# Kernel tuning notes

Hardware: AMD Instinct MI355X
Metric: run time of the kernel (lower is better)

Reference implementation:

```python
import jax, jax.numpy as jnp
import numpy as np

N = 50000
E = 800000
IN_C, HID_C, OUT_C = 64, 96, 32


def setup_inputs() -> dict:
    key = jax.random.key(0)
    ks = jax.random.split(key, 8)
    x = jax.random.normal(ks[0], (N, IN_C), dtype=jnp.float32)
    edge_index = jax.random.randint(ks[1], (2, E), 0, N, dtype=jnp.int32)
    W1 = jax.random.normal(ks[2], (IN_C, HID_C), dtype=jnp.float32) / np.sqrt(IN_C)
    b1 = jnp.zeros((HID_C,), jnp.float32)
    W2 = jax.random.normal(ks[3], (HID_C, HID_C), dtype=jnp.float32) / np.sqrt(HID_C)
    b2 = jnp.zeros((HID_C,), jnp.float32)
    Wfc = jax.random.normal(ks[4], (HID_C, OUT_C), dtype=jnp.float32) / np.sqrt(HID_C)
    bfc = jnp.zeros((OUT_C,), jnp.float32)
    return {"x": x, "edge_index": edge_index, "W1": W1, "b1": b1,
            "W2": W2, "b2": b2, "Wfc": Wfc, "bfc": bfc}


def _gcn_conv(x, src, dst, norm, W, b):
    # x' = D^{-1/2}(A+I)D^{-1/2} (x W) + b   (PyG GCNConv default)
    h = x @ W                                # [N, C_out]
    msg = h[src] * norm[:, None]             # gather + edge scaling
    agg = jax.ops.segment_sum(msg, dst, num_segments=N)  # scatter-add
    return agg + b


def reference(x, edge_index, W1, b1, W2, b2, Wfc, bfc):
    loop = jnp.arange(N, dtype=edge_index.dtype)
    src = jnp.concatenate([edge_index[0], loop])  # add self-loops
    dst = jnp.concatenate([edge_index[1], loop])
    deg = jax.ops.segment_sum(jnp.ones(src.shape[0], jnp.float32), dst,
                              num_segments=N)
    dinv = jax.lax.rsqrt(deg)                # deg >= 1 due to self-loops
    norm = dinv[src] * dinv[dst]             # symmetric normalization per edge
    h = jax.nn.relu(_gcn_conv(x, src, dst, norm, W1, b1))
    # dropout omitted (eval mode / identity)
    h = jax.nn.relu(_gcn_conv(h, src, dst, norm, W2, b2))
    return h @ Wfc + bfc
```

## Files before the change

### kernel.cpp

```cpp
#include <hip/hip_runtime.h>
#include <hip/hip_fp16.h>


constexpr int NN = 50000;
constexpr int NE = 800000;
constexpr int NB = 512;
constexpr int NPB = 98;
constexpr int BCAP = 2048;
constexpr int EPB = 8192;
constexpr int P1B = 1024;
constexpr int NP1 = (NE + EPB - 1) / EPB;

__global__ void zero_bcnt(int* bcnt) {
  int i = threadIdx.x;
  if (i < NB) bcnt[i] = 0;
}

__global__ __launch_bounds__(P1B) void csr_pass1(const int* __restrict__ ei,
                                                 int* __restrict__ bcnt,
                                                 unsigned* __restrict__ bbuf) {
  __shared__ unsigned sorted[EPB];
  __shared__ int hist[NB];
  __shared__ int lofs[NB];
  __shared__ int cursor[NB];
  __shared__ int gbase[NB];
  const int t = threadIdx.x;
  const int e0 = blockIdx.x * EPB;
  const int ecnt = min(EPB, NE - e0);

  for (int i = t; i < NB; i += P1B) hist[i] = 0;
  __syncthreads();

  for (int i = t; i < ecnt; i += P1B) {
    unsigned dst = (unsigned)ei[NE + e0 + i];
    atomicAdd(&hist[dst / NPB], 1);
  }
  __syncthreads();

  if (t < NB) lofs[t] = hist[t];
  __syncthreads();
  for (int off = 1; off < NB; off <<= 1) {
    int v = 0;
    if (t < NB && t >= off) v = lofs[t - off];
    __syncthreads();
    if (t < NB) lofs[t] += v;
    __syncthreads();
  }
  if (t < NB) {
    int ex = lofs[t] - hist[t];
    lofs[t] = ex;
    cursor[t] = ex;
    gbase[t] = atomicAdd(&bcnt[t], hist[t]);
  }
  __syncthreads();

  for (int i = t; i < ecnt; i += P1B) {
    unsigned src = (unsigned)ei[e0 + i];
    unsigned dst = (unsigned)ei[NE + e0 + i];
    unsigned b = dst / NPB;
    unsigned dl = dst - b * NPB;
    int pos = atomicAdd(&cursor[b], 1);
    sorted[pos] = (b << 23) | (dl << 16) | src;
  }
  __syncthreads();

  for (int i = t; i < ecnt; i += P1B) {
    unsigned pw = sorted[i];
    unsigned b = pw >> 23;
    int off_in_b = gbase[b] + (i - lofs[b]);
    if (off_in_b < BCAP)
      bbuf[b * BCAP + off_in_b] = pw & 0x007FFFFFu;
  }
}

__global__ __launch_bounds__(256) void csr_pass2(
    const int* __restrict__ bcnt, const unsigned* __restrict__ bbuf,
    const float* __restrict__ x, int* __restrict__ row_start,
    int* __restrict__ counts, float* __restrict__ dinv,
    __half* __restrict__ u, unsigned short* __restrict__ srcs,
    unsigned* __restrict__ perm) {
  __shared__ int s_red[256];
  __shared__ int s_cnt[128];
  __shared__ int s_scan[128];
  __shared__ int s_cur[128];
  __shared__ float s_dinv[128];
  __shared__ unsigned short s_sorted[BCAP];
  __shared__ int d_hist[64];
  __shared__ int d_cur[64];
  __shared__ int s_permL[NPB];
  const int b = blockIdx.x, t = threadIdx.x;
  const int cnt_b = min(bcnt[b], BCAP);

  int acc = 0;
  for (int j = t; j < b; j += 256) acc += min(bcnt[j], BCAP);
  s_red[t] = acc;
  __syncthreads();
  for (int off = 128; off > 0; off >>= 1) {
    if (t < off) s_red[t] += s_red[t + off];
    __syncthreads();
  }
  const int base = s_red[0];

  if (t < 128) s_cnt[t] = 0;
  __syncthreads();
  for (int i = t; i < cnt_b; i += 256)
    atomicAdd(&s_cnt[bbuf[b * BCAP + i] >> 16], 1);
  __syncthreads();

  if (t < 128) s_scan[t] = s_cnt[t];
  __syncthreads();
  for (int off = 1; off < 128; off <<= 1) {
    int v = 0;
    if (t < 128 && t >= off) v = s_scan[t - off];
    __syncthreads();
    if (t < 128) s_scan[t] += v;
    __syncthreads();
  }
  if (t < 128) s_cur[t] = s_scan[t] - s_cnt[t];

  const int node = b * NPB + t;
  if (t < NPB && node < NN) {
    int c = s_cnt[t];
    row_start[node] = base + s_scan[t] - c;
    counts[node] = c;
    float di = rsqrtf(1.0f + (float)c);
    dinv[node] = di;
    s_dinv[t] = di;
  }
  __syncthreads();

  for (int i = t; i < cnt_b; i += 256) {
    unsigned w = bbuf[b * BCAP + i];
    int pos = atomicAdd(&s_cur[w >> 16], 1);
    s_sorted[pos] = (unsigned short)(w & 0xFFFFu);
  }
  __syncthreads();
  for (int i = t; i < cnt_b; i += 256) srcs[base + i] = s_sorted[i];

  const int na = max(0, min(NN - b * NPB, NPB));
  if (t < 64) d_hist[t] = 0;
  __syncthreads();
  const bool activeN = (t < na);
  const int deg = activeN ? min(s_cnt[t], 63) : 0;
  if (activeN) atomicAdd(&d_hist[deg], 1);
  __syncthreads();
  if (t < 64) d_cur[t] = d_hist[t];
  __syncthreads();
  for (int off = 1; off < 64; off <<= 1) {
    int v = 0;
    if (t < 64 && t >= off) v = d_cur[t - off];
    __syncthreads();
    if (t < 64) d_cur[t] += v;
    __syncthreads();
  }
  if (t < 64) d_cur[t] -= d_hist[t];
  __syncthreads();
  if (activeN) {
    int r = atomicAdd(&d_cur[deg], 1);
    s_permL[r] = t;
  }
  __syncthreads();
  if (t < NPB)
    perm[b * NPB + t] =
        (t < na) ? (unsigned)(b * NPB + s_permL[t]) : 0xFFFFFFFFu;

  const float4* x4 = (const float4*)x;
  for (int i = t; i < NPB * 16; i += 256) {
    int nl = i >> 4, q = i & 15;
    int n = b * NPB + nl;
    if (n < NN) {
      float di = s_dinv[nl];
      float4 v = x4[(size_t)n * 16 + q];
      __half2 h01 = __floats2half2_rn(v.x * di, v.y * di);
      __half2 h23 = __floats2half2_rn(v.z * di, v.w * di);
      uint2 pk;
      pk.x = *(unsigned*)&h01;
      pk.y = *(unsigned*)&h23;
      *(uint2*)(u + (size_t)n * 64 + 4 * q) = pk;
    }
  }
}

template <int C>
__global__ __launch_bounds__(256) void gather_h(
    const unsigned* __restrict__ perm, const int* __restrict__ row_start,
    const int* __restrict__ counts, const unsigned short* __restrict__ srcs,
    const __half* __restrict__ A, float* __restrict__ B) {
  constexpr int QP = C / 8;
  int gid = blockIdx.x * blockDim.x + threadIdx.x;
  if (gid >= NB * NPB * QP) return;
  int i, q;
  if constexpr ((QP & (QP - 1)) == 0) {
    i = gid >> 3;
    q = gid & 7;
  } else {
    i = gid / QP;
    q = gid - i * QP;
  }
  const unsigned node = perm[i];
  if (node == 0xFFFFFFFFu) return;
  const int n = (int)node;
  const uint4* A4 = (const uint4*)A + q;

  float a[8] = {};
  {
    uint4 v = A4[(size_t)n * QP];
    const __half2* h = (const __half2*)&v;
    #pragma unroll
    for (int k = 0; k < 4; ++k) {
      float2 f = __half22float2(h[k]);
      a[2 * k] = f.x;
      a[2 * k + 1] = f.y;
    }
  }
  const int s0 = row_start[n];
  const int cnt = counts[n];
  int p = 0;
  for (; p + 4 <= cnt; p += 4) {
    int sa = srcs[s0 + p + 0];
    int sb = srcs[s0 + p + 1];
    int sc = srcs[s0 + p + 2];
    int sd = srcs[s0 + p + 3];
    uint4 va = A4[(size_t)sa * QP];
    uint4 vb = A4[(size_t)sb * QP];
    uint4 vc = A4[(size_t)sc * QP];
    uint4 vd = A4[(size_t)sd * QP];
    const __half2* ha = (const __half2*)&va;
    const __half2* hb = (const __half2*)&vb;
    const __half2* hc = (const __half2*)&vc;
    const __half2* hd = (const __half2*)&vd;
    #pragma unroll
    for (int k = 0; k < 4; ++k) {
      float2 fa = __half22float2(ha[k]);
      float2 fb = __half22float2(hb[k]);
      float2 fc = __half22float2(hc[k]);
      float2 fd = __half22float2(hd[k]);
      a[2 * k] += (fa.x + fb.x) + (fc.x + fd.x);
      a[2 * k + 1] += (fa.y + fb.y) + (fc.y + fd.y);
    }
  }
  for (; p < cnt; ++p) {
    int s = srcs[s0 + p];
    uint4 v = A4[(size_t)s * QP];
    const __half2* h = (const __half2*)&v;
    #pragma unroll
    for (int k = 0; k < 4; ++k) {
      float2 f = __half22float2(h[k]);
      a[2 * k] += f.x;
      a[2 * k + 1] += f.y;
    }
  }
  float* bp = B + (size_t)n * C + 8 * q;
  *(float4*)bp = make_float4(a[0], a[1], a[2], a[3]);
  *(float4*)(bp + 4) = make_float4(a[4], a[5], a[6], a[7]);
}

template <int K, int M, int MS, int EMODE, int OH>
__global__ __launch_bounds__(256) void sgemm(
    const float* __restrict__ X, const float* __restrict__ W,
    const float* __restrict__ bias, const float* __restrict__ dinv,
    void* __restrict__ outv) {
  constexpr int NS = M / MS;
  constexpr int WQ = MS / 4;
  const int bid = blockIdx.x;
  const int chunk = (NS == 1) ? bid : bid / NS;
  const int slice = (NS == 1) ? 0 : bid - chunk * NS;
  const int c0 = slice * MS;
  const int t = threadIdx.x;
  const int nr = chunk * 256 + t;
  const bool act = nr < NN;
  const int n = act ? nr : NN - 1;

  float acc[MS] = {};
  const float4* __restrict__ xr = (const float4*)(X + (size_t)n * K);
  #pragma unroll 4
  for (int kq = 0; kq < K / 4; ++kq) {
    float4 xv = xr[kq];
    const float xk[4] = {xv.x, xv.y, xv.z, xv.w};
    #pragma unroll
    for (int c = 0; c < 4; ++c) {
      const float* __restrict__ wrow = W + (size_t)(4 * kq + c) * M + c0;
      #pragma unroll
      for (int j = 0; j < MS; ++j)
        acc[j] = fmaf(xk[c], wrow[j], acc[j]);
    }
  }

  if (act) {
    const float di = (EMODE != 3) ? dinv[n] : 0.f;
    #pragma unroll
    for (int j4 = 0; j4 < WQ; ++j4) {
      float b0 = bias[c0 + 4 * j4 + 0], b1 = bias[c0 + 4 * j4 + 1];
      float b2 = bias[c0 + 4 * j4 + 2], b3 = bias[c0 + 4 * j4 + 3];
      float a0 = acc[4 * j4 + 0], a1 = acc[4 * j4 + 1];
      float a2 = acc[4 * j4 + 2], a3 = acc[4 * j4 + 3];
      float4 r;
      if (EMODE == 1) {
        r.x = di * fmaxf(fmaf(di, a0, b0), 0.f);
        r.y = di * fmaxf(fmaf(di, a1, b1), 0.f);
        r.z = di * fmaxf(fmaf(di, a2, b2), 0.f);
        r.w = di * fmaxf(fmaf(di, a3, b3), 0.f);
      } else if (EMODE == 2) {
        r.x = fmaxf(fmaf(di, a0, b0), 0.f);
        r.y = fmaxf(fmaf(di, a1, b1), 0.f);
        r.z = fmaxf(fmaf(di, a2, b2), 0.f);
        r.w = fmaxf(fmaf(di, a3, b3), 0.f);
      } else {
        r.x = a0 + b0; r.y = a1 + b1; r.z = a2 + b2; r.w = a3 + b3;
      }
      if (OH) {
        __half2 h01 = __floats2half2_rn(r.x, r.y);
        __half2 h23 = __floats2half2_rn(r.z, r.w);
        uint2 pk;
        pk.x = *(unsigned*)&h01;
        pk.y = *(unsigned*)&h23;
        *(uint2*)((__half*)outv + (size_t)n * M + c0 + 4 * j4) = pk;
      } else {
        *(float4*)((float*)outv + (size_t)n * M + c0 + 4 * j4) = r;
      }
    }
  }
}

extern "C" void kernel_launch(void* const* d_in, const int* in_sizes, int n_in,
                              void* d_out, int out_size, void* d_ws,
                              size_t ws_size, hipStream_t stream) {
  const float* x   = (const float*)d_in[0];
  const int*   ei  = (const int*)d_in[1];
  const float* W1  = (const float*)d_in[2];
  const float* b1  = (const float*)d_in[3];
  const float* W2  = (const float*)d_in[4];
  const float* b2  = (const float*)d_in[5];
  const float* Wfc = (const float*)d_in[6];
  const float* bfc = (const float*)d_in[7];
  float* out = (float*)d_out;

  float* dinv = (float*)d_ws;
  float* R0 = dinv + 50048;
  float* R1 = R0 + (size_t)NN * 96;
  int* row_start = (int*)(R1 + (size_t)NN * 96);
  int* counts = row_start + 50048;
  int* bcnt = counts + 50048;
  unsigned short* srcs = (unsigned short*)(bcnt + 512);
  unsigned* perm = (unsigned*)(srcs + NE);
  unsigned* bbuf = (unsigned*)R1;
  __half* u_h = (__half*)R0;
  __half* g1_h = (__half*)R0;
  float* B1 = R1;
  float* B2 = R1;
  float* h2 = R0;

  zero_bcnt<<<1, 512, 0, stream>>>(bcnt);
  csr_pass1<<<NP1, P1B, 0, stream>>>(ei, bcnt, bbuf);
  csr_pass2<<<NB, 256, 0, stream>>>(bcnt, bbuf, x, row_start, counts, dinv,
                                    u_h, srcs, perm);

  constexpr int CH = (NN + 255) / 256;

  gather_h<64><<<(NB * NPB * 8 + 255) / 256, 256, 0, stream>>>(
      perm, row_start, counts, srcs, u_h, B1);
  sgemm<64, 96, 32, 1, 1><<<CH * 3, 256, 0, stream>>>(B1, W1, b1, dinv, g1_h);
  gather_h<96><<<(NB * NPB * 12 + 255) / 256, 256, 0, stream>>>(
      perm, row_start, counts, srcs, g1_h, B2);
  sgemm<96, 96, 24, 2, 0><<<CH * 4, 256, 0, stream>>>(B2, W2, b2, dinv, h2);
  sgemm<96, 32, 16, 3, 0><<<CH * 2, 256, 0, stream>>>(h2, Wfc, bfc, dinv, out);
}
```

Measured before the change: 135.3 us.

## Fuse layer-2 GEMM with final FC and shrink CSR pass1 blocks

Replaces the separate layer-2 sgemm and the final fully-connected sgemm with one kernel. It computes relu(dinv*X@W2+b2) for 64 rows into shared memory and then multiplies by Wfc directly, so the 96-wide intermediate h2 never goes through global memory and one launch is dropped. It also retunes csr_pass1 to 4096 edges per block with 256 threads, using a two-bins-per-thread prefix scan. The fused kernel reads W2 and Wfc rows straight from global or cache without tiling, so it may have lower compute efficiency than the templated sgemm.

```diff
diff --git a/kernel.cpp b/kernel.cpp
--- a/kernel.cpp
+++ b/kernel.cpp
@@ -7,8 +7,8 @@
 constexpr int NB = 512;
 constexpr int NPB = 98;
 constexpr int BCAP = 2048;
-constexpr int EPB = 8192;
-constexpr int P1B = 1024;
+constexpr int EPB = 4096;
+constexpr int P1B = 256;
 constexpr int NP1 = (NE + EPB - 1) / EPB;
 
 __global__ void zero_bcnt(int* bcnt) {
@@ -24,6 +24,7 @@
   __shared__ int lofs[NB];
   __shared__ int cursor[NB];
   __shared__ int gbase[NB];
+  __shared__ int psum[P1B];
   const int t = threadIdx.x;
   const int e0 = blockIdx.x * EPB;
   const int ecnt = min(EPB, NE - e0);
@@ -37,20 +38,24 @@
   }
   __syncthreads();
 
-  if (t < NB) lofs[t] = hist[t];
-  __syncthreads();
-  for (int off = 1; off < NB; off <<= 1) {
+  const int h0 = hist[2 * t], h1 = hist[2 * t + 1];
+  psum[t] = h0 + h1;
+  __syncthreads();
+  for (int off = 1; off < P1B; off <<= 1) {
     int v = 0;
-    if (t < NB && t >= off) v = lofs[t - off];
-    __syncthreads();
-    if (t < NB) lofs[t] += v;
-    __syncthreads();
-  }
-  if (t < NB) {
-    int ex = lofs[t] - hist[t];
-    lofs[t] = ex;
-    cursor[t] = ex;
-    gbase[t] = atomicAdd(&bcnt[t], hist[t]);
+    if (t >= off) v = psum[t - off];
+    __syncthreads();
+    psum[t] += v;
+    __syncthreads();
+  }
+  {
+    const int pex = psum[t] - (h0 + h1);
+    lofs[2 * t] = pex;
+    lofs[2 * t + 1] = pex + h0;
+    cursor[2 * t] = pex;
+    cursor[2 * t + 1] = pex + h0;
+    gbase[2 * t] = atomicAdd(&bcnt[2 * t], h0);
+    gbase[2 * t + 1] = atomicAdd(&bcnt[2 * t + 1], h1);
   }
   __syncthreads();
 
@@ -322,6 +327,66 @@
   }
 }
 
+__global__ __launch_bounds__(256) void sgemm2fc(
+    const float* __restrict__ X, const float* __restrict__ W2,
+    const float* __restrict__ b2, const float* __restrict__ Wfc,
+    const float* __restrict__ bfc, const float* __restrict__ dinv,
+    float* __restrict__ out) {
+  __shared__ float sh2[64 * 101];
+  const int t = threadIdx.x;
+  const int nl = t >> 2;
+  const int c0 = (t & 3) * 24;
+  const int nr = blockIdx.x * 64 + nl;
+  const bool act = nr < NN;
+  const int n = act ? nr : NN - 1;
+
+  float acc[24] = {};
+  const float4* __restrict__ xr = (const float4*)(X + (size_t)n * 96);
+  #pragma unroll 4
+  for (int kq = 0; kq < 24; ++kq) {
+    float4 xv = xr[kq];
+    const float xk[4] = {xv.x, xv.y, xv.z, xv.w};
+    #pragma unroll
+    for (int c = 0; c < 4; ++c) {
+      const float* __restrict__ wrow = W2 + (size_t)(4 * kq + c) * 96 + c0;
+      #pragma unroll
+      for (int j = 0; j < 24; ++j)
+        acc[j] = fmaf(xk[c], wrow[j], acc[j]);
+    }
+  }
+  {
+    const float di = dinv[n];
+    float* sp = sh2 + nl * 101 + c0;
+    #pragma unroll
+    for (int j = 0; j < 24; ++j)
+      sp[j] = fmaxf(fmaf(di, acc[j], b2[c0 + j]), 0.f);
+  }
+  __syncthreads();
+
+  const int nl2 = t & 63;
+  const int m0 = (t >> 6) * 8;
+  const int nr2 = blockIdx.x * 64 + nl2;
+  float o[8] = {};
+  const float* __restrict__ hrow = sh2 + nl2 * 101;
+  #pragma unroll 8
+  for (int k = 0; k < 96; ++k) {
+    const float hk = hrow[k];
+    const float* __restrict__ wr = Wfc + (size_t)k * 32 + m0;
+    #pragma unroll
+    for (int j = 0; j < 8; ++j) o[j] = fmaf(hk, wr[j], o[j]);
+  }
+  if (nr2 < NN) {
+    float* op = out + (size_t)nr2 * 32 + m0;
+    float4 r0, r1;
+    r0.x = o[0] + bfc[m0 + 0]; r0.y = o[1] + bfc[m0 + 1];
+    r0.z = o[2] + bfc[m0 + 2]; r0.w = o[3] + bfc[m0 + 3];
+    r1.x = o[4] + bfc[m0 + 4]; r1.y = o[5] + bfc[m0 + 5];
+    r1.z = o[6] + bfc[m0 + 6]; r1.w = o[7] + bfc[m0 + 7];
+    *(float4*)op = r0;
+    *(float4*)(op + 4) = r1;
+  }
+}
+
 extern "C" void kernel_launch(void* const* d_in, const int* in_sizes, int n_in,
                               void* d_out, int out_size, void* d_ws,
                               size_t ws_size, hipStream_t stream) {
@@ -348,7 +413,6 @@
   __half* g1_h = (__half*)R0;
   float* B1 = R1;
   float* B2 = R1;
-  float* h2 = R0;
 
   zero_bcnt<<<1, 512, 0, stream>>>(bcnt);
   csr_pass1<<<NP1, P1B, 0, stream>>>(ei, bcnt, bbuf);
@@ -362,6 +426,6 @@
   sgemm<64, 96, 32, 1, 1><<<CH * 3, 256, 0, stream>>>(B1, W1, b1, dinv, g1_h);
   gather_h<96><<<(NB * NPB * 12 + 255) / 256, 256, 0, stream>>>(
       perm, row_start, counts, srcs, g1_h, B2);
-  sgemm<96, 96, 24, 2, 0><<<CH * 4, 256, 0, stream>>>(B2, W2, b2, dinv, h2);
-  sgemm<96, 32, 16, 3, 0><<<CH * 2, 256, 0, stream>>>(h2, Wfc, bfc, dinv, out);
-}
+  sgemm2fc<<<(NN + 63) / 64, 256, 0, stream>>>(B2, W2, b2, Wfc, bfc, dinv,
+                                               out);
+}
```

Result: slower. 204.6 us (+51.2%).
